# Kernel optimization log

Hardware: AMD Instinct MI355X
Metric: run time of the kernel (lower is better)

The kernel has to match this reference:

```python
import jax, jax.numpy as jnp
import numpy as np

# config constants (match init_kwargs)
C = 1024
NH = 16
HS = C // NH
CHUNK = 64          # attn_chunk_size
TOPK = 32           # attn_topk
WINDOW = 4096       # kv_cache_window_size
MIN_KV = 16384      # min_kv_cache_size
MAX_KV = 32768      # max_kv_cache_size
SHORT = 4096        # short_sequence_criteria
CT = 65536          # incoming kv-cache length


def setup_inputs() -> dict:
    key = jax.random.key(0)
    ks = jax.random.split(key, 7)
    s = 1.0 / np.sqrt(C)
    return {
        "x": jax.random.normal(ks[0], (C,), jnp.float32),
        "k_cache": jax.random.normal(ks[1], (1, CT, C), jnp.float32),
        "v_cache": jax.random.normal(ks[2], (1, CT, C), jnp.float32),
        "Wr": jax.random.normal(ks[3], (C, C), jnp.float32) * s,
        "Wk": jax.random.normal(ks[4], (C, C), jnp.float32) * s,
        "Wv": jax.random.normal(ks[5], (C, C), jnp.float32) * s,
        "Wo": jax.random.normal(ks[6], (C, C), jnp.float32) * s,
    }


def _split_heads(t):  # (1, T, C) -> (1, NH, T, HS)
    return t.reshape(1, t.shape[1], NH, HS).transpose(0, 2, 1, 3)


def _update_kv_cache(q, k_cache, v_cache):
    # q: (1,1,C); caches: (1,CT,C). CT > MIN_KV so compression runs.
    past = CT - WINDOW
    kp = _split_heads(k_cache[:, :past])          # (1,NH,past,HS)
    vp = _split_heads(v_cache[:, :past])
    qh = _split_heads(q)                          # (1,NH,1,HS)
    scores = jnp.einsum("bhqd,bhkd->bhqk", qh, kp) / np.sqrt(HS)
    w = jax.nn.softmax(scores, axis=-1)           # (1,NH,1,past)
    vote = w.sum(axis=-2)                         # (1,NH,past)
    keep = MIN_KV - WINDOW                        # per-head tokens kept
    _, idx = jax.lax.top_k(vote, keep)            # (1,NH,keep), descending vote order
    kpc = jnp.take_along_axis(kp, idx[..., None], axis=2)  # (1,NH,keep,HS)
    vpc = jnp.take_along_axis(vp, idx[..., None], axis=2)
    kpc = kpc.transpose(0, 2, 1, 3).reshape(1, keep, C)
    vpc = vpc.transpose(0, 2, 1, 3).reshape(1, keep, C)
    k_new = jnp.concatenate([kpc, k_cache[:, past:]], axis=1)  # (1, MIN_KV, C)
    v_new = jnp.concatenate([vpc, v_cache[:, past:]], axis=1)
    return k_new, v_new


def reference(x, k_cache, v_cache, Wr, Wk, Wv, Wo):
    x2 = x[None, None, :]                         # (1,1,C)
    q = x2 @ Wr.T
    k = x2 @ Wk.T
    v = x2 @ Wv.T

    # CT > MAX_KV -> compress cache (eviction via attention vote per head)
    k_cache, v_cache = _update_kv_cache(q, k_cache, v_cache)
    CT2 = k_cache.shape[1]                        # MIN_KV = 16384 > SHORT -> sparse path

    num_chunks = CT2 // CHUNK
    kc = k_cache.reshape(1, num_chunks, CHUNK, C)
    vc = v_cache.reshape(1, num_chunks, CHUNK, C)
    chunk_key = kc.mean(axis=2)                   # (1,num_chunks,C)
    chunk_score = jnp.einsum("bqc,bkc->bqk", q, chunk_key)
    _, tidx = jax.lax.top_k(chunk_score[0, 0], TOPK)  # (TOPK,)
    topk_k = kc[:, tidx].reshape(1, TOPK * CHUNK, C)
    topk_v = vc[:, tidx].reshape(1, TOPK * CHUNK, C)

    k_comb = jnp.concatenate([topk_k, k], axis=1)  # (1, TOPK*CHUNK+1, C)
    v_comb = jnp.concatenate([topk_v, v], axis=1)

    qh = _split_heads(q)                          # (1,NH,1,HS)
    kh = _split_heads(k_comb)
    vh = _split_heads(v_comb)
    attn = jax.nn.softmax(
        jnp.einsum("bhqd,bhkd->bhqk", qh, kh) / np.sqrt(HS), axis=-1)
    y = jnp.einsum("bhqk,bhkd->bhqd", attn, vh)   # (1,NH,1,HS)
    y = y.transpose(0, 2, 1, 3).reshape(C)
    y = y @ Wo.T
    return y
```

## Files before the change

### kernel.cpp

```cpp
#include <hip/hip_runtime.h>
#include <stdint.h>

#define C      1024
#define NH     16
#define HS     64
#define CT     65536
#define PAST   61440
#define KEEP   12288
#define NCOMP  192
#define NSEL   32
#define NBINS  16384
#define CAP    16384

__device__ __forceinline__ unsigned int desc_key(float f) {
    unsigned int b = __float_as_uint(f);
    return (b >> 31) ? b : (~b & 0x7FFFFFFFu);
}
__device__ __forceinline__ float u_to_f(unsigned int u) {
    unsigned int b = (u & 0x80000000u) ? u : (0x7FFFFFFFu - u);
    return __uint_as_float(b);
}
__device__ __forceinline__ int bin_of(float s, float hi, float scale) {
    int b = (int)((hi - s) * scale);
    return b < 0 ? 0 : (b > NBINS - 1 ? NBINS - 1 : b);
}

__global__ void k_proj(const float* __restrict__ x, const float* __restrict__ Wr,
                       const float* __restrict__ Wk, const float* __restrict__ Wv,
                       float* __restrict__ q, float* __restrict__ kn, float* __restrict__ vn) {
    int w = blockIdx.x * (blockDim.x >> 6) + (threadIdx.x >> 6);
    int lane = threadIdx.x & 63;
    int mat = w >> 10, row = w & 1023;
    const float* W = (mat == 0) ? Wr : (mat == 1) ? Wk : Wv;
    const float4* Wrow = (const float4*)(W + (size_t)row * C);
    const float4* x4 = (const float4*)x;
    float acc = 0.f;
#pragma unroll
    for (int i = 0; i < 4; ++i) {
        float4 a = Wrow[i * 64 + lane];
        float4 b = x4[i * 64 + lane];
        acc += a.x * b.x + a.y * b.y + a.z * b.z + a.w * b.w;
    }
#pragma unroll
    for (int off = 32; off; off >>= 1) acc += __shfl_xor(acc, off);
    if (lane == 0) { (mat == 0 ? q : (mat == 1 ? kn : vn))[row] = acc; }
}

__global__ void k_scores(const float* __restrict__ kc, const float* __restrict__ q,
                         float* __restrict__ s) {
    int wid = blockIdx.x * (blockDim.x >> 6) + (threadIdx.x >> 6);
    int lane = threadIdx.x & 63;
    int nw = gridDim.x * (blockDim.x >> 6);
    const float4* q4 = (const float4*)q;
    float4 qv[4];
#pragma unroll
    for (int i = 0; i < 4; ++i) qv[i] = q4[i * 64 + lane];
    for (int t = wid; t < CT; t += nw) {
        const float4* row = (const float4*)(kc + (size_t)t * C);
        float acc[4];
#pragma unroll
        for (int i = 0; i < 4; ++i) {
            float4 a = row[i * 64 + lane];
            acc[i] = a.x * qv[i].x + a.y * qv[i].y + a.z * qv[i].z + a.w * qv[i].w;
        }
#pragma unroll
        for (int off = 8; off; off >>= 1) {
#pragma unroll
            for (int i = 0; i < 4; ++i) acc[i] += __shfl_xor(acc[i], off);
        }
        if ((lane & 15) == 0) {
            int g = lane >> 4;
#pragma unroll
            for (int i = 0; i < 4; ++i) s[(size_t)(4 * i + g) * CT + t] = acc[i];
        }
    }
}

__global__ __launch_bounds__(1024) void s0_init(unsigned* __restrict__ hist,
                                                unsigned* __restrict__ umin,
                                                unsigned* __restrict__ umax) {
    int id = blockIdx.x * 1024 + threadIdx.x;
    if (id < 16 * NBINS) hist[id] = 0;
    if (blockIdx.x == 0) {
        if (threadIdx.x < 16) umin[threadIdx.x] = 0xFFFFFFFFu;
        else if (threadIdx.x < 32) umax[threadIdx.x - 16] = 0u;
    }
}

__global__ void s0b_minmax(const float* __restrict__ s, unsigned* __restrict__ umin,
                           unsigned* __restrict__ umax) {
    __shared__ unsigned smin[4], smax[4];
    int h = blockIdx.x >> 4, seg = blockIdx.x & 15;
    int tid = threadIdx.x, lane = tid & 63, wave = tid >> 6;
    const float* sh = s + (size_t)h * CT + seg * 3840;
    unsigned mn = 0xFFFFFFFFu, mx = 0u;
    for (int i = tid; i < 3840; i += 256) {
        unsigned u = desc_key(sh[i]);
        mn = mn < u ? mn : u;
        mx = mx > u ? mx : u;
    }
#pragma unroll
    for (int off = 32; off; off >>= 1) {
        unsigned a = __shfl_xor(mn, off), b = __shfl_xor(mx, off);
        mn = mn < a ? mn : a;
        mx = mx > b ? mx : b;
    }
    if (lane == 0) { smin[wave] = mn; smax[wave] = mx; }
    __syncthreads();
    if (tid == 0) {
        mn = smin[0]; mx = smax[0];
        for (int w = 1; w < 4; ++w) {
            mn = mn < smin[w] ? mn : smin[w];
            mx = mx > smax[w] ? mx : smax[w];
        }
        atomicMin(&umin[h], mn);
        atomicMax(&umax[h], mx);
    }
}

__global__ void s0c_params(const unsigned* __restrict__ umin, const unsigned* __restrict__ umax,
                           float* __restrict__ hiArr, float* __restrict__ scArr) {
    int h = threadIdx.x;
    if (h >= 16) return;
    float hi = u_to_f(umin[h]);
    float lo = u_to_f(umax[h]);
    float r = hi - lo;
    scArr[h] = (r > 0.f) ? (float)(NBINS - 1) / r : 0.f;
    hiArr[h] = hi;
}

__global__ __launch_bounds__(1024) void s1_hist(const float* __restrict__ s,
                                                unsigned* __restrict__ hist,
                                                const float* __restrict__ hiArr,
                                                const float* __restrict__ scArr) {
    __shared__ unsigned lh[NBINS];
    int h = blockIdx.x >> 2, seg = blockIdx.x & 3;
    int tid = threadIdx.x;
    for (int i = tid; i < NBINS; i += 1024) lh[i] = 0;
    __syncthreads();
    float hi = hiArr[h], sc = scArr[h];
    const float* sh = s + (size_t)h * CT + seg * 15360;
    for (int i = tid; i < 15360; i += 1024)
        atomicAdd(&lh[bin_of(sh[i], hi, sc)], 1u);
    __syncthreads();
    unsigned* gh = hist + h * NBINS;
    for (int i = tid; i < NBINS; i += 1024) {
        unsigned c = lh[i];
        if (c) atomicAdd(&gh[i], c);
    }
}

__global__ __launch_bounds__(1024) void s2_scan(unsigned* __restrict__ base,
                                                unsigned* __restrict__ Tarr) {
    __shared__ unsigned wsum[16];
    int h = blockIdx.x, tid = threadIdx.x, lane = tid & 63, wave = tid >> 6;
    unsigned* B = base + h * NBINS;
    unsigned cnt[16];
    unsigned loc = 0;
    int b0 = tid * 16;
#pragma unroll
    for (int k = 0; k < 16; ++k) { cnt[k] = B[b0 + k]; loc += cnt[k]; }
    unsigned run = loc;
#pragma unroll
    for (int off = 1; off < 64; off <<= 1) {
        unsigned n = __shfl_up(run, off);
        if (lane >= off) run += n;
    }
    if (lane == 63) wsum[wave] = run;
    __syncthreads();
    if (wave == 0 && lane < 16) {
        unsigned v = wsum[lane];
#pragma unroll
        for (int off = 1; off < 16; off <<= 1) {
            unsigned n = __shfl_up(v, off);
            if (lane >= off) v += n;
        }
        wsum[lane] = v;
    }
    __syncthreads();
    unsigned r = run - loc + (wave ? wsum[wave - 1] : 0u);
#pragma unroll
    for (int k = 0; k < 16; ++k) {
        unsigned c = cnt[k];
        B[b0 + k] = r;
        unsigned inc = r + c;
        if (r < KEEP && inc >= KEEP) Tarr[h] = (unsigned)(b0 + k);
        r = inc;
    }
}

__global__ __launch_bounds__(1024) void s3_scatter(const float* __restrict__ s,
                                                   unsigned* __restrict__ base,
                                                   const unsigned* __restrict__ Tarr,
                                                   unsigned* __restrict__ G,
                                                   const float* __restrict__ hiArr,
                                                   const float* __restrict__ scArr) {
    int h = blockIdx.x / 60, seg = blockIdx.x % 60;
    int t = seg * 1024 + threadIdx.x;
    float v = s[(size_t)h * CT + t];
    int b = bin_of(v, hiArr[h], scArr[h]);
    if ((unsigned)b <= Tarr[h]) {
        unsigned pos = atomicAdd(&base[h * NBINS + b], 1u);
        if (pos < CAP) G[h * CAP + pos] = (unsigned)t;
    }
}

__global__ __launch_bounds__(1024) void s4_rank(const float* __restrict__ s,
                                                const unsigned* __restrict__ base,
                                                const unsigned* __restrict__ Tarr,
                                                const unsigned* __restrict__ G,
                                                const float* __restrict__ hiArr,
                                                const float* __restrict__ scArr,
                                                unsigned short* __restrict__ stok) {
    int h = blockIdx.x >> 4, seg = blockIdx.x & 15;
    int p = seg * 1024 + threadIdx.x;
    unsigned T = Tarr[h];
    unsigned ncand = base[h * NBINS + T];
    if (ncand > CAP) ncand = CAP;
    if (p >= (int)ncand) return;
    unsigned tok = G[h * CAP + p];
    const float* sh = s + (size_t)h * CT;
    float v = sh[tok];
    unsigned u = desc_key(v);
    int b = bin_of(v, hiArr[h], scArr[h]);
    unsigned start = b ? base[h * NBINS + b - 1] : 0u;
    unsigned end = base[h * NBINS + b];
    if (end > CAP) end = CAP;
    unsigned rank = start;
    for (unsigned j = start; j < end; ++j) {
        unsigned t2 = G[h * CAP + j];
        unsigned u2 = desc_key(sh[t2]);
        rank += (u2 < u || (u2 == u && t2 < tok)) ? 1u : 0u;
    }
    if (rank < KEEP) stok[h * KEEP + rank] = (unsigned short)tok;
}

__global__ void k_chunkscore(const float* __restrict__ s,
                             const unsigned short* __restrict__ stok,
                             float* __restrict__ cs) {
    int c = blockIdx.x;
    int tid = threadIdx.x;
    __shared__ float red[256];
    float acc = 0.f;
    for (int p = tid; p < 64 * NH; p += 256) {
        int j = p & 63, hh = p >> 6;
        int t = (c < NCOMP) ? (int)stok[hh * KEEP + c * 64 + j]
                            : (PAST + (c - NCOMP) * 64 + j);
        acc += s[(size_t)hh * CT + t];
    }
    red[tid] = acc;
    __syncthreads();
    for (int st = 128; st; st >>= 1) {
        if (tid < st) red[tid] += red[tid + st];
        __syncthreads();
    }
    if (tid == 0) cs[c] = red[0] * (1.f / 64.f);
}

__global__ void k_top32(const float* __restrict__ cs, unsigned int* __restrict__ sel) {
    __shared__ unsigned long long key[256];
    int tid = threadIdx.x;
    unsigned int u = desc_key(cs[tid]);
    key[tid] = ((unsigned long long)u << 32) | (unsigned int)tid;
    __syncthreads();
    for (unsigned k = 2; k <= 256; k <<= 1) {
        for (unsigned j = k >> 1; j > 0; j >>= 1) {
            unsigned ixj = tid ^ j;
            if (ixj > (unsigned)tid) {
                unsigned long long a = key[tid], b = key[ixj];
                bool up = ((tid & k) == 0);
                bool sw = up ? (a > b) : (a < b);
                if (sw) { key[tid] = b; key[ixj] = a; }
            }
            __syncthreads();
        }
    }
    if (tid < NSEL) sel[tid] = (unsigned int)(key[tid] & 0xFFFFFFFFull);
}

__global__ void k_attn_part(const float* __restrict__ s, const float* __restrict__ vc,
                            const unsigned short* __restrict__ stok,
                            const unsigned int* __restrict__ sel,
                            float* __restrict__ part) {
    int h = blockIdx.x >> 5, ci = blockIdx.x & 31;
    int tid = threadIdx.x;
    int g = tid >> 2, b3 = tid & 3;
    int c = (int)sel[ci];
    int t = (c < NCOMP) ? (int)stok[h * KEEP + c * 64 + g]
                        : (PAST + (c - NCOMP) * 64 + g);
    __shared__ float sc[64];
    __shared__ float ex[64];
    __shared__ float vbuf[64][65];
    if (b3 == 0) sc[g] = s[(size_t)h * CT + t] * 0.125f;
    __syncthreads();
    float m = -1e30f;
    for (int j = 0; j < 64; ++j) m = fmaxf(m, sc[j]);
    float e = expf(sc[g] - m);
    const float4* vrow = (const float4*)(vc + (size_t)t * C + h * HS);
#pragma unroll
    for (int it = 0; it < 4; ++it) {
        float4 vv = vrow[it * 4 + b3];
        int d0 = it * 16 + b3 * 4;
        vbuf[g][d0 + 0] = e * vv.x;
        vbuf[g][d0 + 1] = e * vv.y;
        vbuf[g][d0 + 2] = e * vv.z;
        vbuf[g][d0 + 3] = e * vv.w;
    }
    if (b3 == 0) ex[g] = e;
    __syncthreads();
    if (tid < 64) {
        float acc = 0.f;
        for (int g2 = 0; g2 < 64; ++g2) acc += vbuf[g2][tid];
        float* P = part + (size_t)(h * 32 + ci) * 68;
        P[2 + tid] = acc;
        if (tid == 0) {
            float es = 0.f;
            for (int g2 = 0; g2 < 64; ++g2) es += ex[g2];
            P[0] = m;
            P[1] = es;
        }
    }
}

__global__ void k_attn_fin(const float* __restrict__ part, const float* __restrict__ q,
                           const float* __restrict__ kn, const float* __restrict__ vn,
                           float* __restrict__ y) {
    int h = blockIdx.x;
    int lane = threadIdx.x;
    float qd = q[h * HS + lane] * kn[h * HS + lane];
#pragma unroll
    for (int off = 32; off; off >>= 1) qd += __shfl_xor(qd, off);
    float a_new = qd * 0.125f;
    const float* P0 = part + (size_t)h * 32 * 68;
    float m = a_new;
    for (int ci = 0; ci < 32; ++ci) m = fmaxf(m, P0[ci * 68]);
    float den = expf(a_new - m);
    float acc = den * vn[h * HS + lane];
    for (int ci = 0; ci < 32; ++ci) {
        float w = expf(P0[ci * 68] - m);
        den += w * P0[ci * 68 + 1];
        acc += w * P0[ci * 68 + 2 + lane];
    }
    y[h * HS + lane] = acc / den;
}

__global__ void k_out(const float* __restrict__ Wo, const float* __restrict__ y,
                      float* __restrict__ out) {
    int w = blockIdx.x * (blockDim.x >> 6) + (threadIdx.x >> 6);
    int lane = threadIdx.x & 63;
    const float4* Wrow = (const float4*)(Wo + (size_t)w * C);
    const float4* y4 = (const float4*)y;
    float acc = 0.f;
#pragma unroll
    for (int i = 0; i < 4; ++i) {
        float4 a = Wrow[i * 64 + lane];
        float4 b = y4[i * 64 + lane];
        acc += a.x * b.x + a.y * b.y + a.z * b.z + a.w * b.w;
    }
#pragma unroll
    for (int off = 32; off; off >>= 1) acc += __shfl_xor(acc, off);
    if (lane == 0) out[w] = acc;
}

extern "C" void kernel_launch(void* const* d_in, const int* in_sizes, int n_in,
                              void* d_out, int out_size, void* d_ws, size_t ws_size,
                              hipStream_t stream) {
    const float* x  = (const float*)d_in[0];
    const float* kc = (const float*)d_in[1];
    const float* vc = (const float*)d_in[2];
    const float* Wr = (const float*)d_in[3];
    const float* Wk = (const float*)d_in[4];
    const float* Wv = (const float*)d_in[5];
    const float* Wo = (const float*)d_in[6];
    float* out = (float*)d_out;
    char* ws = (char*)d_ws;

    float* q    = (float*)(ws + 0);
    float* kn   = (float*)(ws + 8192);
    float* vn   = (float*)(ws + 16384);
    float* y    = (float*)(ws + 24576);
    float* cs   = (float*)(ws + 32768);
    unsigned int* sel = (unsigned int*)(ws + 40960);
    float* part = (float*)(ws + 49152);
    unsigned short* stok = (unsigned short*)(ws + 196608);
    unsigned* umin  = (unsigned*)(ws + 655360);
    unsigned* umax  = (unsigned*)(ws + 655360 + 64);
    float*    hiArr = (float*)(ws + 655360 + 128);
    float*    scArr = (float*)(ws + 655360 + 192);
    unsigned* Tarr  = (unsigned*)(ws + 655360 + 256);
    float* s = (float*)(ws + 1048576);
    unsigned* base = (unsigned*)(ws + 5242880);
    unsigned* G    = (unsigned*)(ws + 6291456);

    s0_init<<<256, 1024, 0, stream>>>(base, umin, umax);
    k_proj<<<768, 256, 0, stream>>>(x, Wr, Wk, Wv, q, kn, vn);
    k_scores<<<2048, 256, 0, stream>>>(kc, q, s);
    s0b_minmax<<<256, 256, 0, stream>>>(s, umin, umax);
    s0c_params<<<1, 64, 0, stream>>>(umin, umax, hiArr, scArr);
    s1_hist<<<64, 1024, 0, stream>>>(s, base, hiArr, scArr);
    s2_scan<<<16, 1024, 0, stream>>>(base, Tarr);
    s3_scatter<<<960, 1024, 0, stream>>>(s, base, Tarr, G, hiArr, scArr);
    s4_rank<<<256, 1024, 0, stream>>>(s, base, Tarr, G, hiArr, scArr, stok);
    k_chunkscore<<<256, 256, 0, stream>>>(s, stok, cs);
    k_top32<<<1, 256, 0, stream>>>(cs, sel);
    k_attn_part<<<512, 256, 0, stream>>>(s, vc, stok, sel, part);
    k_attn_fin<<<16, 64, 0, stream>>>(part, q, kn, vn, y);
    k_out<<<256, 256, 0, stream>>>(Wo, y, out);
}
```

Before: 142.9 us.

## Fuse per-head top-k selection pipeline and chunk scoring into one block-per-head kernel

Replaces seven kernels (init, min/max, params, histogram, scan, scatter, rank, chunk-score) with a single k_select kernel that runs one 1024-thread block per head. Min/max, histogram, scan, scatter and rank all happen in shared memory, and the bin count drops to 8192. Candidates are packed as 64-bit key|token so ranking compares packed values directly. Chunk scores are accumulated as fixed-point integers via atomics during ranking, so results are deterministic. This removes many launches and global-memory round trips, but uses only 16 blocks, which limits parallelism on a large GPU.

Result: slower. 165.4 us (+15.8%).

```diff
diff --git a/kernel.cpp b/kernel.cpp
--- a/kernel.cpp
+++ b/kernel.cpp
@@ -9,8 +9,7 @@
 #define KEEP   12288
 #define NCOMP  192
 #define NSEL   32
-#define NBINS  16384
-#define CAP    16384
+#define NB     8192
 
 __device__ __forceinline__ unsigned int desc_key(float f) {
     unsigned int b = __float_as_uint(f);
@@ -22,12 +21,14 @@
 }
 __device__ __forceinline__ int bin_of(float s, float hi, float scale) {
     int b = (int)((hi - s) * scale);
-    return b < 0 ? 0 : (b > NBINS - 1 ? NBINS - 1 : b);
+    return b < 0 ? 0 : (b > NB - 1 ? NB - 1 : b);
 }
 
 __global__ void k_proj(const float* __restrict__ x, const float* __restrict__ Wr,
                        const float* __restrict__ Wk, const float* __restrict__ Wv,
-                       float* __restrict__ q, float* __restrict__ kn, float* __restrict__ vn) {
+                       float* __restrict__ q, float* __restrict__ kn, float* __restrict__ vn,
+                       unsigned long long* __restrict__ cs_fix) {
+    if (blockIdx.x == 0 && threadIdx.x < 256) cs_fix[threadIdx.x] = 0ull;
     int w = blockIdx.x * (blockDim.x >> 6) + (threadIdx.x >> 6);
     int lane = threadIdx.x & 63;
     int mat = w >> 10, row = w & 1023;
@@ -76,192 +77,133 @@
     }
 }
 
-__global__ __launch_bounds__(1024) void s0_init(unsigned* __restrict__ hist,
-                                                unsigned* __restrict__ umin,
-                                                unsigned* __restrict__ umax) {
-    int id = blockIdx.x * 1024 + threadIdx.x;
-    if (id < 16 * NBINS) hist[id] = 0;
-    if (blockIdx.x == 0) {
-        if (threadIdx.x < 16) umin[threadIdx.x] = 0xFFFFFFFFu;
-        else if (threadIdx.x < 32) umax[threadIdx.x - 16] = 0u;
-    }
-}
-
-__global__ void s0b_minmax(const float* __restrict__ s, unsigned* __restrict__ umin,
-                           unsigned* __restrict__ umax) {
-    __shared__ unsigned smin[4], smax[4];
-    int h = blockIdx.x >> 4, seg = blockIdx.x & 15;
-    int tid = threadIdx.x, lane = tid & 63, wave = tid >> 6;
-    const float* sh = s + (size_t)h * CT + seg * 3840;
-    unsigned mn = 0xFFFFFFFFu, mx = 0u;
-    for (int i = tid; i < 3840; i += 256) {
-        unsigned u = desc_key(sh[i]);
-        mn = mn < u ? mn : u;
-        mx = mx > u ? mx : u;
+__global__ __launch_bounds__(1024) void k_select(const float* __restrict__ s,
+                                                 unsigned long long* __restrict__ G,
+                                                 unsigned short* __restrict__ stok,
+                                                 unsigned long long* __restrict__ cs_fix) {
+    __shared__ unsigned hist[NB];
+    __shared__ float redA[16], redB[16];
+    __shared__ unsigned wsum[16];
+    __shared__ unsigned long long csl[NCOMP];
+    __shared__ float sh_hi, sh_sc;
+    __shared__ unsigned sh_T;
+
+    const int h = blockIdx.x, tid = threadIdx.x;
+    const int lane = tid & 63, wave = tid >> 6;
+    const float* sh = s + (size_t)h * CT;
+    unsigned long long* Gh = G + (size_t)h * 65536;
+
+    if (tid < NCOMP) csl[tid] = 0ull;
+
+    float mn = 3.4e38f, mx = -3.4e38f;
+    for (int t = tid; t < PAST; t += 1024) {
+        float v = sh[t];
+        mn = fminf(mn, v); mx = fmaxf(mx, v);
     }
 #pragma unroll
     for (int off = 32; off; off >>= 1) {
-        unsigned a = __shfl_xor(mn, off), b = __shfl_xor(mx, off);
-        mn = mn < a ? mn : a;
-        mx = mx > b ? mx : b;
-    }
-    if (lane == 0) { smin[wave] = mn; smax[wave] = mx; }
+        mn = fminf(mn, __shfl_xor(mn, off));
+        mx = fmaxf(mx, __shfl_xor(mx, off));
+    }
+    if (lane == 0) { redA[wave] = mn; redB[wave] = mx; }
+    for (int i = tid; i < NB; i += 1024) hist[i] = 0;
     __syncthreads();
     if (tid == 0) {
-        mn = smin[0]; mx = smax[0];
-        for (int w = 1; w < 4; ++w) {
-            mn = mn < smin[w] ? mn : smin[w];
-            mx = mx > smax[w] ? mx : smax[w];
-        }
-        atomicMin(&umin[h], mn);
-        atomicMax(&umax[h], mx);
-    }
-}
-
-__global__ void s0c_params(const unsigned* __restrict__ umin, const unsigned* __restrict__ umax,
-                           float* __restrict__ hiArr, float* __restrict__ scArr) {
-    int h = threadIdx.x;
-    if (h >= 16) return;
-    float hi = u_to_f(umin[h]);
-    float lo = u_to_f(umax[h]);
-    float r = hi - lo;
-    scArr[h] = (r > 0.f) ? (float)(NBINS - 1) / r : 0.f;
-    hiArr[h] = hi;
-}
-
-__global__ __launch_bounds__(1024) void s1_hist(const float* __restrict__ s,
-                                                unsigned* __restrict__ hist,
-                                                const float* __restrict__ hiArr,
-                                                const float* __restrict__ scArr) {
-    __shared__ unsigned lh[NBINS];
-    int h = blockIdx.x >> 2, seg = blockIdx.x & 3;
-    int tid = threadIdx.x;
-    for (int i = tid; i < NBINS; i += 1024) lh[i] = 0;
-    __syncthreads();
-    float hi = hiArr[h], sc = scArr[h];
-    const float* sh = s + (size_t)h * CT + seg * 15360;
-    for (int i = tid; i < 15360; i += 1024)
-        atomicAdd(&lh[bin_of(sh[i], hi, sc)], 1u);
-    __syncthreads();
-    unsigned* gh = hist + h * NBINS;
-    for (int i = tid; i < NBINS; i += 1024) {
-        unsigned c = lh[i];
-        if (c) atomicAdd(&gh[i], c);
-    }
-}
-
-__global__ __launch_bounds__(1024) void s2_scan(unsigned* __restrict__ base,
-                                                unsigned* __restrict__ Tarr) {
-    __shared__ unsigned wsum[16];
-    int h = blockIdx.x, tid = threadIdx.x, lane = tid & 63, wave = tid >> 6;
-    unsigned* B = base + h * NBINS;
-    unsigned cnt[16];
-    unsigned loc = 0;
-    int b0 = tid * 16;
-#pragma unroll
-    for (int k = 0; k < 16; ++k) { cnt[k] = B[b0 + k]; loc += cnt[k]; }
-    unsigned run = loc;
-#pragma unroll
-    for (int off = 1; off < 64; off <<= 1) {
-        unsigned n = __shfl_up(run, off);
-        if (lane >= off) run += n;
-    }
-    if (lane == 63) wsum[wave] = run;
-    __syncthreads();
-    if (wave == 0 && lane < 16) {
-        unsigned v = wsum[lane];
-#pragma unroll
-        for (int off = 1; off < 16; off <<= 1) {
-            unsigned n = __shfl_up(v, off);
-            if (lane >= off) v += n;
-        }
-        wsum[lane] = v;
-    }
-    __syncthreads();
-    unsigned r = run - loc + (wave ? wsum[wave - 1] : 0u);
-#pragma unroll
-    for (int k = 0; k < 16; ++k) {
-        unsigned c = cnt[k];
-        B[b0 + k] = r;
-        unsigned inc = r + c;
-        if (r < KEEP && inc >= KEEP) Tarr[h] = (unsigned)(b0 + k);
-        r = inc;
-    }
-}
-
-__global__ __launch_bounds__(1024) void s3_scatter(const float* __restrict__ s,
-                                                   unsigned* __restrict__ base,
-                                                   const unsigned* __restrict__ Tarr,
-                                                   unsigned* __restrict__ G,
-                                                   const float* __restrict__ hiArr,
-                                                   const float* __restrict__ scArr) {
-    int h = blockIdx.x / 60, seg = blockIdx.x % 60;
-    int t = seg * 1024 + threadIdx.x;
-    float v = s[(size_t)h * CT + t];
-    int b = bin_of(v, hiArr[h], scArr[h]);
-    if ((unsigned)b <= Tarr[h]) {
-        unsigned pos = atomicAdd(&base[h * NBINS + b], 1u);
-        if (pos < CAP) G[h * CAP + pos] = (unsigned)t;
-    }
-}
-
-__global__ __launch_bounds__(1024) void s4_rank(const float* __restrict__ s,
-                                                const unsigned* __restrict__ base,
-                                                const unsigned* __restrict__ Tarr,
-                                                const unsigned* __restrict__ G,
-                                                const float* __restrict__ hiArr,
-                                                const float* __restrict__ scArr,
-                                                unsigned short* __restrict__ stok) {
-    int h = blockIdx.x >> 4, seg = blockIdx.x & 15;
-    int p = seg * 1024 + threadIdx.x;
-    unsigned T = Tarr[h];
-    unsigned ncand = base[h * NBINS + T];
-    if (ncand > CAP) ncand = CAP;
-    if (p >= (int)ncand) return;
-    unsigned tok = G[h * CAP + p];
-    const float* sh = s + (size_t)h * CT;
-    float v = sh[tok];
-    unsigned u = desc_key(v);
-    int b = bin_of(v, hiArr[h], scArr[h]);
-    unsigned start = b ? base[h * NBINS + b - 1] : 0u;
-    unsigned end = base[h * NBINS + b];
-    if (end > CAP) end = CAP;
-    unsigned rank = start;
-    for (unsigned j = start; j < end; ++j) {
-        unsigned t2 = G[h * CAP + j];
-        unsigned u2 = desc_key(sh[t2]);
-        rank += (u2 < u || (u2 == u && t2 < tok)) ? 1u : 0u;
-    }
-    if (rank < KEEP) stok[h * KEEP + rank] = (unsigned short)tok;
-}
-
-__global__ void k_chunkscore(const float* __restrict__ s,
-                             const unsigned short* __restrict__ stok,
-                             float* __restrict__ cs) {
-    int c = blockIdx.x;
-    int tid = threadIdx.x;
-    __shared__ float red[256];
-    float acc = 0.f;
-    for (int p = tid; p < 64 * NH; p += 256) {
-        int j = p & 63, hh = p >> 6;
-        int t = (c < NCOMP) ? (int)stok[hh * KEEP + c * 64 + j]
-                            : (PAST + (c - NCOMP) * 64 + j);
-        acc += s[(size_t)hh * CT + t];
-    }
-    red[tid] = acc;
-    __syncthreads();
-    for (int st = 128; st; st >>= 1) {
-        if (tid < st) red[tid] += red[tid + st];
+        float lo = redA[0], hi2 = redB[0];
+        for (int w = 1; w < 16; ++w) { lo = fminf(lo, redA[w]); hi2 = fmaxf(hi2, redB[w]); }
+        float r = hi2 - lo;
+        sh_hi = hi2;
+        sh_sc = (r > 0.f) ? (float)(NB - 1) / r : 0.f;
+    }
+    __syncthreads();
+    const float hi = sh_hi, sc = sh_sc;
+
+    for (int t = tid; t < PAST; t += 1024)
+        atomicAdd(&hist[bin_of(sh[t], hi, sc)], 1u);
+    __syncthreads();
+
+    {
+        unsigned cnt[8]; unsigned loc = 0; int b0 = tid * 8;
+#pragma unroll
+        for (int k = 0; k < 8; ++k) { cnt[k] = hist[b0 + k]; loc += cnt[k]; }
+        unsigned run = loc;
+#pragma unroll
+        for (int off = 1; off < 64; off <<= 1) {
+            unsigned n = __shfl_up(run, off);
+            if (lane >= off) run += n;
+        }
+        if (lane == 63) wsum[wave] = run;
         __syncthreads();
-    }
-    if (tid == 0) cs[c] = red[0] * (1.f / 64.f);
-}
-
-__global__ void k_top32(const float* __restrict__ cs, unsigned int* __restrict__ sel) {
+        if (wave == 0 && lane < 16) {
+            unsigned v = wsum[lane];
+#pragma unroll
+            for (int off = 1; off < 16; off <<= 1) {
+                unsigned n = __shfl_up(v, off);
+                if (lane >= off) v += n;
+            }
+            wsum[lane] = v;
+        }
+        __syncthreads();
+        unsigned r = run - loc + (wave ? wsum[wave - 1] : 0u);
+#pragma unroll
+        for (int k = 0; k < 8; ++k) {
+            unsigned c = cnt[k];
+            hist[b0 + k] = r;
+            unsigned inc = r + c;
+            if (r < KEEP && inc >= KEEP) sh_T = (unsigned)(b0 + k);
+            r = inc;
+        }
+    }
+    __syncthreads();
+    const unsigned T = sh_T;
+
+    for (int t = tid; t < PAST; t += 1024) {
+        float v = sh[t];
+        int b = bin_of(v, hi, sc);
+        if ((unsigned)b <= T) {
+            unsigned pos = atomicAdd(&hist[b], 1u);
+            Gh[pos] = ((unsigned long long)desc_key(v) << 16) | (unsigned)t;
+        }
+    }
+    __syncthreads();
+
+    unsigned ncand = hist[T];
+    for (int p = tid; p < (int)ncand; p += 1024) {
+        unsigned long long pk = Gh[p];
+        unsigned u = (unsigned)(pk >> 16);
+        float v = u_to_f(u);
+        int b = bin_of(v, hi, sc);
+        unsigned start = b ? hist[b - 1] : 0u;
+        unsigned end = hist[b];
+        unsigned rank = start;
+        for (unsigned j = start; j < end; ++j) rank += (Gh[j] < pk) ? 1u : 0u;
+        if (rank < KEEP) {
+            stok[h * KEEP + rank] = (unsigned short)(pk & 0xFFFFull);
+            long long f = llrintf(v * 16777216.f);
+            atomicAdd(&csl[rank >> 6], (unsigned long long)f);
+        }
+    }
+
+#pragma unroll
+    for (int k = 0; k < 4; ++k) {
+        int i = tid + k * 1024;
+        float v = sh[PAST + i];
+        long long f = llrintf(v * 16777216.f);
+#pragma unroll
+        for (int off = 32; off; off >>= 1) f += __shfl_xor(f, off);
+        if (lane == 0) atomicAdd(&cs_fix[NCOMP + wave + k * 16], (unsigned long long)f);
+    }
+    __syncthreads();
+    if (tid < NCOMP) atomicAdd(&cs_fix[tid], csl[tid]);
+}
+
+__global__ void k_top32(const unsigned long long* __restrict__ cs_fix,
+                        unsigned int* __restrict__ sel) {
     __shared__ unsigned long long key[256];
     int tid = threadIdx.x;
-    unsigned int u = desc_key(cs[tid]);
-    key[tid] = ((unsigned long long)u << 32) | (unsigned int)tid;
+    long long v = (long long)cs_fix[tid];
+    unsigned long long bb = (unsigned long long)(v + (1ll << 45));
+    key[tid] = (((1ull << 46) - bb) << 8) | (unsigned)tid;
     __syncthreads();
     for (unsigned k = 2; k <= 256; k <<= 1) {
         for (unsigned j = k >> 1; j > 0; j >>= 1) {
@@ -275,7 +217,7 @@
             __syncthreads();
         }
     }
-    if (tid < NSEL) sel[tid] = (unsigned int)(key[tid] & 0xFFFFFFFFull);
+    if (tid < NSEL) sel[tid] = (unsigned int)(key[tid] & 0xFFull);
 }
 
 __global__ void k_attn_part(const float* __restrict__ s, const float* __restrict__ vc,
@@ -288,14 +230,14 @@
     int c = (int)sel[ci];
     int t = (c < NCOMP) ? (int)stok[h * KEEP + c * 64 + g]
                         : (PAST + (c - NCOMP) * 64 + g);
-    __shared__ float sc[64];
+    __shared__ float scm[64];
     __shared__ float ex[64];
     __shared__ float vbuf[64][65];
-    if (b3 == 0) sc[g] = s[(size_t)h * CT + t] * 0.125f;
+    if (b3 == 0) scm[g] = s[(size_t)h * CT + t] * 0.125f;
     __syncthreads();
     float m = -1e30f;
-    for (int j = 0; j < 64; ++j) m = fmaxf(m, sc[j]);
-    float e = expf(sc[g] - m);
+    for (int j = 0; j < 64; ++j) m = fmaxf(m, scm[j]);
+    float e = expf(scm[g] - m);
     const float4* vrow = (const float4*)(vc + (size_t)t * C + h * HS);
 #pragma unroll
     for (int it = 0; it < 4; ++it) {
@@ -379,30 +321,17 @@
     float* kn   = (float*)(ws + 8192);
     float* vn   = (float*)(ws + 16384);
     float* y    = (float*)(ws + 24576);
-    float* cs   = (float*)(ws + 32768);
+    unsigned long long* cs_fix = (unsigned long long*)(ws + 32768);
     unsigned int* sel = (unsigned int*)(ws + 40960);
     float* part = (float*)(ws + 49152);
     unsigned short* stok = (unsigned short*)(ws + 196608);
-    unsigned* umin  = (unsigned*)(ws + 655360);
-    unsigned* umax  = (unsigned*)(ws + 655360 + 64);
-    float*    hiArr = (float*)(ws + 655360 + 128);
-    float*    scArr = (float*)(ws + 655360 + 192);
-    unsigned* Tarr  = (unsigned*)(ws + 655360 + 256);
     float* s = (float*)(ws + 1048576);
-    unsigned* base = (unsigned*)(ws + 5242880);
-    unsigned* G    = (unsigned*)(ws + 6291456);
-
-    s0_init<<<256, 1024, 0, stream>>>(base, umin, umax);
-    k_proj<<<768, 256, 0, stream>>>(x, Wr, Wk, Wv, q, kn, vn);
+    unsigned long long* G = (unsigned long long*)(ws + 8388608);
+
+    k_proj<<<768, 256, 0, stream>>>(x, Wr, Wk, Wv, q, kn, vn, cs_fix);
     k_scores<<<2048, 256, 0, stream>>>(kc, q, s);
-    s0b_minmax<<<256, 256, 0, stream>>>(s, umin, umax);
-    s0c_params<<<1, 64, 0, stream>>>(umin, umax, hiArr, scArr);
-    s1_hist<<<64, 1024, 0, stream>>>(s, base, hiArr, scArr);
-    s2_scan<<<16, 1024, 0, stream>>>(base, Tarr);
-    s3_scatter<<<960, 1024, 0, stream>>>(s, base, Tarr, G, hiArr, scArr);
-    s4_rank<<<256, 1024, 0, stream>>>(s, base, Tarr, G, hiArr, scArr, stok);
-    k_chunkscore<<<256, 256, 0, stream>>>(s, stok, cs);
-    k_top32<<<1, 256, 0, stream>>>(cs, sel);
+    k_select<<<16, 1024, 0, stream>>>(s, G, stok, cs_fix);
+    k_top32<<<1, 256, 0, stream>>>(cs_fix, sel);
     k_attn_part<<<512, 256, 0, stream>>>(s, vc, stok, sel, part);
     k_attn_fin<<<16, 64, 0, stream>>>(part, q, kn, vn, y);
     k_out<<<256, 256, 0, stream>>>(Wo, y, out);
```
